# Performance work log

Measured on AMD Instinct MI355X. Metric: run time of the kernel, lower is better.

Reference implementation:

```python
import jax, jax.numpy as jnp
import numpy as np
from jax import lax

B, L, LQ, D_IN, ET, H, INIT_EMBED = 16, 256, 64, 32, 128, 4, 8
DIM = 2 * D_IN          # attention value/feature dim (x concat mask)
ETK = ET // H           # per-head time-embedding dim


def _lin(key, fan_in, shape):
    b = 1.0 / np.sqrt(fan_in)
    return jax.random.uniform(key, shape, jnp.float32, -b, b)


def setup_inputs() -> dict:
    key = jax.random.key(0)
    ks = jax.random.split(key, 24)
    inp = {
        "x": jax.random.normal(ks[0], (B, L, D_IN), jnp.float32),
        "time_steps": jnp.sort(jax.random.uniform(ks[1], (B, L), jnp.float32), axis=-1),
        "mask": (jax.random.uniform(ks[2], (B, L, D_IN)) > 0.5).astype(jnp.float32),
        "query": jnp.linspace(0.0, 1.0, LQ, dtype=jnp.float32),
        # time embedding: Linear(1,1) and Linear(1, ET-1)
        "w_lin": _lin(ks[3], 1, (1,)), "b_lin": _lin(ks[4], 1, (1,)),
        "w_per": _lin(ks[5], 1, (ET - 1,)), "b_per": _lin(ks[6], 1, (ET - 1,)),
        # attention projections (stored as (in,out))
        "Wq": _lin(ks[7], ET, (ET, ET)), "bq": _lin(ks[8], ET, (ET,)),
        "Wk": _lin(ks[9], ET, (ET, ET)), "bk": _lin(ks[10], ET, (ET,)),
        "Wo": _lin(ks[11], H * DIM, (H * DIM, ET)), "bo": _lin(ks[12], H * DIM, (ET,)),
        # vanilla RNN (tanh)
        "W_ih": _lin(ks[13], ET, (ET, ET)), "b_ih": _lin(ks[14], ET, (ET,)),
        "W_hh": _lin(ks[15], ET, (ET, ET)), "b_hh": _lin(ks[16], ET, (ET,)),
        "r1_w": _lin(ks[17], ET, (ET, 128)), "r1_b": _lin(ks[17], ET, (128,)),
        "r2_w": _lin(ks[18], 128, (128, 128)), "r2_b": _lin(ks[18], 128, (128,)),
        "r3_w": _lin(ks[19], 128, (128, ET)), "r3_b": _lin(ks[19], 128, (ET,)),
        "r4_w": _lin(ks[20], ET, (ET, INIT_EMBED)), "r4_b": _lin(ks[20], ET, (INIT_EMBED,)),
    }
    return inp


def reference(x, time_steps, mask, query,
              w_lin, b_lin, w_per, b_per,
              Wq, bq, Wk, bk, Wo, bo,
              W_ih, b_ih, W_hh, b_hh,
              r1_w, r1_b, r2_w, r2_b, r3_w, r3_b, r4_w, r4_b):
    def time_embed(tt):  # (...,) -> (..., ET)
        tt = tt[..., None]
        return jnp.concatenate([tt * w_lin + b_lin,
                                jnp.sin(tt * w_per + b_per)], axis=-1)

    xc = jnp.concatenate([x, mask], axis=-1)          # (B,L,DIM) value
    m2 = jnp.concatenate([mask, mask], axis=-1)       # (B,L,DIM)

    kemb = time_embed(time_steps)                     # (B,L,ET)
    qemb = time_embed(query)                          # (LQ,ET)

    q = (qemb @ Wq + bq).reshape(LQ, H, ETK).transpose(1, 0, 2)       # (H,LQ,ETK)
    k = (kemb @ Wk + bk).reshape(B, L, H, ETK).transpose(0, 2, 1, 3)  # (B,H,L,ETK)

    scores = jnp.einsum('hqe,bhke->bhqk', q, k) / np.sqrt(ETK)        # (B,H,LQ,L)
    # per-feature mask broadcast: (B,H,LQ,L,DIM)
    s5 = jnp.where(m2[:, None, None, :, :] == 0, -1e9, scores[..., None])
    p = jax.nn.softmax(s5, axis=-2)                   # softmax over keys L
    att = jnp.einsum('bhqkd,bkd->bhqd', p, xc)        # (B,H,LQ,DIM)
    att = att.transpose(0, 2, 1, 3).reshape(B, LQ, H * DIM)
    out = att @ Wo + bo                               # (B,LQ,ET)

    # vanilla tanh RNN, return final hidden state
    def step(h, xt):
        h = jnp.tanh(xt @ W_ih + b_ih + h @ W_hh + b_hh)
        return h, None
    h0 = jnp.zeros((B, ET), out.dtype)
    hT, _ = lax.scan(step, h0, out.transpose(1, 0, 2))  # scan over LQ

    y = hT @ r1_w + r1_b
    y = y @ r2_w + r2_b
    y = y @ r3_w + r3_b
    y = y @ r4_w + r4_b                               # (B, INIT_EMBED)
    return y
```

## Files before the change

### kernel.cpp

```cpp
#include <hip/hip_runtime.h>
#include <hip/hip_bf16.h>


#define NB 16
#define NL 256
#define NLQ 64
#define NDIN 32
#define NET 128
#define NH 4
#define NETK 32

#define HPAD 136
#define PAD(i) ((i) + 4 * ((i) >> 6))

__global__ __launch_bounds__(128) void k_embed_proj(
    const float* __restrict__ ts, const float* __restrict__ query,
    const float* __restrict__ mask,
    const float* __restrict__ w_lin, const float* __restrict__ b_lin,
    const float* __restrict__ w_per, const float* __restrict__ b_per,
    const float* __restrict__ Wk, const float* __restrict__ bk,
    const float* __restrict__ Wq, const float* __restrict__ bq,
    float* __restrict__ kproj, float* __restrict__ qproj,
    unsigned* __restrict__ mbg) {
  __shared__ __align__(16) float emb[8 * NET];
  int g = blockIdx.x;
  int j = threadIdx.x;

  if (g >= 520) {
    int b = g - 520;
#pragma unroll
    for (int half = 0; half < 2; half++) {
      int r = j + 128 * half;
      const float4* mr4 = (const float4*)(mask + (size_t)(b * NL + r) * NDIN);
      unsigned bits = 0;
#pragma unroll
      for (int u = 0; u < 8; u++) {
        float4 m = mr4[u];
        bits |= (m.x != 0.f ? 1u : 0u) << (4 * u);
        bits |= (m.y != 0.f ? 1u : 0u) << (4 * u + 1);
        bits |= (m.z != 0.f ? 1u : 0u) << (4 * u + 2);
        bits |= (m.w != 0.f ? 1u : 0u) << (4 * u + 3);
      }
      mbg[b * NL + r] = bits;
    }
    return;
  }

  bool isQ = (g >= 512);
  int base = (isQ ? g - 512 : g) * 8;
  float wl_ = w_lin[0], bl_ = b_lin[0];
  float wp = (j > 0) ? w_per[j - 1] : 0.f;
  float bp = (j > 0) ? b_per[j - 1] : 0.f;
#pragma unroll
  for (int rr = 0; rr < 8; rr++) {
    float t = isQ ? query[base + rr] : ts[base + rr];
    emb[rr * NET + j] = (j == 0) ? (t * wl_ + bl_) : sinf(t * wp + bp);
  }
  __syncthreads();
  const float* W = isQ ? Wq : Wk;
  float bias = isQ ? bq[j] : bk[j];
  float acc[8];
#pragma unroll
  for (int rr = 0; rr < 8; rr++) acc[rr] = bias;
#pragma unroll 2
  for (int i = 0; i < NET; i += 4) {
    float w0 = W[(size_t)i * NET + j];
    float w1 = W[(size_t)(i + 1) * NET + j];
    float w2 = W[(size_t)(i + 2) * NET + j];
    float w3 = W[(size_t)(i + 3) * NET + j];
#pragma unroll
    for (int rr = 0; rr < 8; rr++) {
      float4 e4 = *(const float4*)&emb[rr * NET + i];
      acc[rr] += e4.x * w0 + e4.y * w1 + e4.z * w2 + e4.w * w3;
    }
  }
  float* dst = isQ ? qproj : kproj;
#pragma unroll
  for (int rr = 0; rr < 8; rr++) dst[(size_t)(base + rr) * NET + j] = acc[rr];
}

__global__ __launch_bounds__(256) void k_attn(
    const float* __restrict__ x, const unsigned* __restrict__ mbg,
    const float* __restrict__ qproj, const float* __restrict__ kproj,
    float* __restrict__ att) {
  const float SC = 0.17677669529663687f;
  int blk = blockIdx.x;
  int qg = blk & 15;
  int h  = (blk >> 4) & 3;
  int b  = blk >> 6;
  int t  = threadIdx.x;

  __shared__ __align__(16) float es4[NL * 4];
  __shared__ float part[3 * 32 * 9];

  {
    int k = t;
    float kr[NETK];
    const float4* kp =
        (const float4*)(kproj + (size_t)(b * NL + k) * NET + h * NETK);
#pragma unroll
    for (int i = 0; i < 8; i++) {
      float4 v = kp[i];
      kr[4 * i] = v.x; kr[4 * i + 1] = v.y;
      kr[4 * i + 2] = v.z; kr[4 * i + 3] = v.w;
    }
    float ev[4];
#pragma unroll
    for (int qq = 0; qq < 4; qq++) {
      const float* qv = qproj + (size_t)(qg * 4 + qq) * NET + h * NETK;
      float s0 = 0.f, s1 = 0.f;
#pragma unroll
      for (int i = 0; i < NETK; i += 2) {
        s0 += qv[i] * kr[i];
        s1 += qv[i + 1] * kr[i + 1];
      }
      ev[qq] = __expf((s0 + s1) * SC);
    }
    *(float4*)&es4[k * 4] = make_float4(ev[0], ev[1], ev[2], ev[3]);
  }
  __syncthreads();

  int kq = t >> 5, c = t & 31;
  float den[4] = {0.f, 0.f, 0.f, 0.f};
  float num[4] = {0.f, 0.f, 0.f, 0.f};
  float sumx = 0.f;
  {
    const float* xb = x + (size_t)b * NL * NDIN;
    const unsigned* mbb = mbg + b * NL;
    int k0 = kq * 32;
#pragma unroll 4
    for (int kk = 0; kk < 32; kk++) {
      int k = k0 + kk;
      float4 e4 = *(const float4*)&es4[k * 4];
      float xv = xb[(size_t)k * NDIN + c];
      float mv = ((mbb[k] >> c) & 1u) ? 1.f : 0.f;
      sumx += xv;
      float e0 = e4.x * mv, e1 = e4.y * mv, e2 = e4.z * mv, e3 = e4.w * mv;
      den[0] += e0; num[0] += e0 * xv;
      den[1] += e1; num[1] += e1 * xv;
      den[2] += e2; num[2] += e2 * xv;
      den[3] += e3; num[3] += e3 * xv;
    }
  }
  sumx += __shfl_xor(sumx, 32, 64);
#pragma unroll
  for (int q = 0; q < 4; q++) {
    den[q] += __shfl_xor(den[q], 32, 64);
    num[q] += __shfl_xor(num[q], 32, 64);
  }
  {
    int w = t >> 6, lane = t & 63;
    if (w > 0 && lane < 32) {
      float* p = &part[((w - 1) * 32 + c) * 9];
#pragma unroll
      for (int q = 0; q < 4; q++) { p[q] = den[q]; p[4 + q] = num[q]; }
      p[8] = sumx;
    }
  }
  __syncthreads();

  if (t < 32) {
#pragma unroll
    for (int ww = 0; ww < 3; ww++) {
      const float* p = &part[(ww * 32 + t) * 9];
#pragma unroll
      for (int q = 0; q < 4; q++) { den[q] += p[q]; num[q] += p[4 + q]; }
      sumx += p[8];
    }
    float meanx = sumx * (1.f / 256.f);
#pragma unroll
    for (int qq = 0; qq < 4; qq++) {
      bool any = (den[qq] > 0.f);
      float* ao =
          att + (size_t)(((b * NLQ + qg * 4 + qq) * NH) + h) * 64;
      ao[t]      = any ? (num[qq] / den[qq]) : meanx;
      ao[32 + t] = any ? 1.f : 0.f;
    }
  }
}

__global__ __launch_bounds__(128) void k_out_xw(
    const float* __restrict__ att,
    const float* __restrict__ Wo, const float* __restrict__ bo,
    const float* __restrict__ Wih, const float* __restrict__ bih,
    const float* __restrict__ bhh, float* __restrict__ XW) {
  int r = blockIdx.x;
  int j = threadIdx.x;
  __shared__ __align__(16) float arow[NH * 64];
  __shared__ __align__(16) float orow[NET];
  arow[j]       = att[(size_t)r * 256 + j];
  arow[j + 128] = att[(size_t)r * 256 + 128 + j];
  __syncthreads();
  float a0 = bo[j], a1 = 0.f, a2 = 0.f, a3 = 0.f;
#pragma unroll 4
  for (int u = 0; u < 256; u += 4) {
    float4 av = *(const float4*)&arow[u];
    a0 += av.x * Wo[(size_t)u * NET + j];
    a1 += av.y * Wo[(size_t)(u + 1) * NET + j];
    a2 += av.z * Wo[(size_t)(u + 2) * NET + j];
    a3 += av.w * Wo[(size_t)(u + 3) * NET + j];
  }
  orow[j] = (a0 + a1) + (a2 + a3);
  __syncthreads();
  float b0 = bih[j] + bhh[j], b1 = 0.f, b2 = 0.f, b3 = 0.f;
#pragma unroll 4
  for (int e = 0; e < NET; e += 4) {
    float4 ov = *(const float4*)&orow[e];
    b0 += ov.x * Wih[(size_t)e * NET + j];
    b1 += ov.y * Wih[(size_t)(e + 1) * NET + j];
    b2 += ov.z * Wih[(size_t)(e + 2) * NET + j];
    b3 += ov.w * Wih[(size_t)(e + 3) * NET + j];
  }
  XW[(size_t)r * NET + j] = (b0 + b1) + (b2 + b3);
}

__device__ __forceinline__ void layer128(const float* src_lds,
                                         const float* __restrict__ W,
                                         const float* __restrict__ bvec,
                                         float* dst_lds, int j, int s) {
  const float4* h4 = (const float4*)(src_lds + s * 68);
  float a0 = 0.f, a1 = 0.f, a2 = 0.f, a3 = 0.f;
#pragma unroll
  for (int i = 0; i < 16; i++) {
    float4 hv = h4[i];
    int base = (s * 64 + 4 * i) * NET + j;
    a0 += hv.x * W[base];
    a1 += hv.y * W[base + NET];
    a2 += hv.z * W[base + 2 * NET];
    a3 += hv.w * W[base + 3 * NET];
  }
  float acc = (a0 + a1) + (a2 + a3);
  acc += __shfl_xor(acc, 1, 64);
  if (s == 0) dst_lds[PAD(j)] = acc + bvec[j];
}

__global__ __launch_bounds__(256, 1) void k_rnn(
    const float* __restrict__ XW, const float* __restrict__ Whh,
    const float* __restrict__ r1w, const float* __restrict__ r1b,
    const float* __restrict__ r2w, const float* __restrict__ r2b,
    const float* __restrict__ r3w, const float* __restrict__ r3b,
    const float* __restrict__ r4w, const float* __restrict__ r4b,
    float* __restrict__ out) {
  int b = blockIdx.x;
  int tid = threadIdx.x;
  int s = tid & 1;
  int j = tid >> 1;
  __shared__ float xwl[NLQ * NET];
  __shared__ float hb[2][HPAD];
  __shared__ float tmp[HPAD];

  {
    const float4* src = (const float4*)(XW + (size_t)b * NLQ * NET);
    float4* dst = (float4*)xwl;
#pragma unroll
    for (int u = 0; u < 8; u++) dst[tid + 256 * u] = src[tid + 256 * u];
  }
  float w[64];
#pragma unroll
  for (int i = 0; i < 64; i++) w[i] = Whh[(s * 64 + i) * NET + j];

  if (tid < 128) hb[0][PAD(tid)] = 0.f;
  __syncthreads();

  for (int t = 0; t < NLQ; t++) {
    float xwv = xwl[t * NET + j];
    const float4* h4 = (const float4*)&hb[t & 1][s * 68];
    float a0 = 0.f, a1 = 0.f, a2 = 0.f, a3 = 0.f;
#pragma unroll
    for (int i = 0; i < 16; i++) {
      float4 hv = h4[i];
      a0 += hv.x * w[4 * i];
      a1 += hv.y * w[4 * i + 1];
      a2 += hv.z * w[4 * i + 2];
      a3 += hv.w * w[4 * i + 3];
    }
    float acc = (a0 + a1) + (a2 + a3);
    acc += __shfl_xor(acc, 1, 64);
    if (s == 0) {
      float z = acc + xwv;
      float e2 = __expf(2.f * z);
      hb[(t + 1) & 1][PAD(j)] = 1.f - 2.f / (e2 + 1.f);
    }
    __syncthreads();
  }

  layer128(hb[0], r1w, r1b, tmp, j, s);
  __syncthreads();
  layer128(tmp, r2w, r2b, hb[1], j, s);
  __syncthreads();
  layer128(hb[1], r3w, r3b, hb[0], j, s);
  __syncthreads();
  if (tid < 64) {
    int jj = tid >> 3, p = tid & 7;
    float y = 0.f;
#pragma unroll
    for (int i = 0; i < 16; i++) {
      int ii = p * 16 + i;
      y += hb[0][PAD(ii)] * r4w[ii * 8 + jj];
    }
    y += __shfl_xor(y, 1, 64);
    y += __shfl_xor(y, 2, 64);
    y += __shfl_xor(y, 4, 64);
    if (p == 0) out[b * 8 + jj] = y + r4b[jj];
  }
}

extern "C" void kernel_launch(void* const* d_in, const int* in_sizes, int n_in,
                              void* d_out, int out_size, void* d_ws, size_t ws_size,
                              hipStream_t stream) {
  const float* x     = (const float*)d_in[0];
  const float* ts    = (const float*)d_in[1];
  const float* mask  = (const float*)d_in[2];
  const float* query = (const float*)d_in[3];
  const float* w_lin = (const float*)d_in[4];
  const float* b_lin = (const float*)d_in[5];
  const float* w_per = (const float*)d_in[6];
  const float* b_per = (const float*)d_in[7];
  const float* Wq    = (const float*)d_in[8];
  const float* bq    = (const float*)d_in[9];
  const float* Wk    = (const float*)d_in[10];
  const float* bk    = (const float*)d_in[11];
  const float* Wo    = (const float*)d_in[12];
  const float* bo    = (const float*)d_in[13];
  const float* Wih   = (const float*)d_in[14];
  const float* bih   = (const float*)d_in[15];
  const float* Whh   = (const float*)d_in[16];
  const float* bhh   = (const float*)d_in[17];
  const float* r1w   = (const float*)d_in[18];
  const float* r1b   = (const float*)d_in[19];
  const float* r2w   = (const float*)d_in[20];
  const float* r2b   = (const float*)d_in[21];
  const float* r3w   = (const float*)d_in[22];
  const float* r3b   = (const float*)d_in[23];
  const float* r4w   = (const float*)d_in[24];
  const float* r4b   = (const float*)d_in[25];
  float* out = (float*)d_out;

  float* ws    = (float*)d_ws;
  float* kproj = ws;
  float* qproj = ws + 524288;
  float* att   = ws + 532480;
  float* XW    = ws + 794624;
  unsigned* mbg = (unsigned*)(ws + 925696);

  k_embed_proj<<<536, 128, 0, stream>>>(
      ts, query, mask, w_lin, b_lin, w_per, b_per, Wk, bk, Wq, bq,
      kproj, qproj, mbg);
  k_attn<<<NB * NH * 16, 256, 0, stream>>>(x, mbg, qproj, kproj, att);
  k_out_xw<<<NB * NLQ, 128, 0, stream>>>(att, Wo, bo, Wih, bih, bhh, XW);
  k_rnn<<<NB, 256, 0, stream>>>(XW, Whh, r1w, r1b, r2w, r2b, r3w, r3b,
                                r4w, r4b, out);
}
```

Baseline: 178.9 us.

## Fuse all stages into one cooperative persistent kernel with grid syncs

Replaces the four-kernel pipeline with a single cooperative kernel that runs embedding/projection, attention plus the output and input-to-hidden projections, and the RNN with the regressor as phases separated by grid.sync. Attention is regrouped per (batch, query) so all heads are done in one block, and the attention output goes straight into the Wo/Wih projections through shared memory, so the att buffer round-trip and the separate k_out_xw launch are gone. The aim is to cut kernel launch gaps and intermediate global traffic. In exchange, the sequential RNN phase runs on only 16 blocks while the rest of the grid sits idle, grid-wide barriers add cost, and each block now recomputes all four heads' scores for its query. The old multi-kernel path is kept as a fallback if the cooperative launch fails.

New measurement: 415.8 us. 2.32x slower.

```diff
diff --git a/kernel.cpp b/kernel.cpp
--- a/kernel.cpp
+++ b/kernel.cpp
@@ -1,5 +1,8 @@
 #include <hip/hip_runtime.h>
 #include <hip/hip_bf16.h>
+#include <hip/hip_cooperative_groups.h>
+
+namespace cg = cooperative_groups;
 
 
 #define NB 16
@@ -12,6 +15,293 @@
 
 #define HPAD 136
 #define PAD(i) ((i) + 4 * ((i) >> 6))
+
+__device__ __forceinline__ void layer128(const float* src_lds,
+                                         const float* __restrict__ W,
+                                         const float* __restrict__ bvec,
+                                         float* dst_lds, int j, int s) {
+  const float4* h4 = (const float4*)(src_lds + s * 68);
+  float a0 = 0.f, a1 = 0.f, a2 = 0.f, a3 = 0.f;
+#pragma unroll
+  for (int i = 0; i < 16; i++) {
+    float4 hv = h4[i];
+    int base = (s * 64 + 4 * i) * NET + j;
+    a0 += hv.x * W[base];
+    a1 += hv.y * W[base + NET];
+    a2 += hv.z * W[base + 2 * NET];
+    a3 += hv.w * W[base + 3 * NET];
+  }
+  float acc = (a0 + a1) + (a2 + a3);
+  acc += __shfl_xor(acc, 1, 64);
+  if (s == 0) dst_lds[PAD(j)] = acc + bvec[j];
+}
+
+__device__ __forceinline__ void embed_unit256(
+    float* emb, const float* __restrict__ tsrc, int base,
+    float wl, float bl, float wp, float bp,
+    const float* __restrict__ W, float bias,
+    float* __restrict__ dst, int t) {
+  int j = t & 127, half = t >> 7;
+  __syncthreads();
+#pragma unroll
+  for (int rr = 0; rr < 4; rr++) {
+    int r = half * 4 + rr;
+    float tv = tsrc[base + r];
+    emb[r * NET + j] = (j == 0) ? (tv * wl + bl) : sinf(tv * wp + bp);
+  }
+  __syncthreads();
+  float acc[4] = {bias, bias, bias, bias};
+#pragma unroll 2
+  for (int i = 0; i < NET; i += 4) {
+    float w0 = W[(size_t)i * NET + j];
+    float w1 = W[(size_t)(i + 1) * NET + j];
+    float w2 = W[(size_t)(i + 2) * NET + j];
+    float w3 = W[(size_t)(i + 3) * NET + j];
+#pragma unroll
+    for (int rr = 0; rr < 4; rr++) {
+      float4 e4 = *(const float4*)&emb[(half * 4 + rr) * NET + i];
+      acc[rr] += e4.x * w0 + e4.y * w1 + e4.z * w2 + e4.w * w3;
+    }
+  }
+#pragma unroll
+  for (int rr = 0; rr < 4; rr++)
+    dst[(size_t)(base + half * 4 + rr) * NET + j] = acc[rr];
+}
+
+__global__ __launch_bounds__(256, 4) void k_mega(
+    const float* __restrict__ x, const float* __restrict__ ts,
+    const float* __restrict__ mask, const float* __restrict__ query,
+    const float* __restrict__ w_lin, const float* __restrict__ b_lin,
+    const float* __restrict__ w_per, const float* __restrict__ b_per,
+    const float* __restrict__ Wq, const float* __restrict__ bq,
+    const float* __restrict__ Wk, const float* __restrict__ bk,
+    const float* __restrict__ Wo, const float* __restrict__ bo,
+    const float* __restrict__ Wih, const float* __restrict__ bih,
+    const float* __restrict__ Whh, const float* __restrict__ bhh,
+    const float* __restrict__ r1w, const float* __restrict__ r1b,
+    const float* __restrict__ r2w, const float* __restrict__ r2b,
+    const float* __restrict__ r3w, const float* __restrict__ r3b,
+    const float* __restrict__ r4w, const float* __restrict__ r4b,
+    float* __restrict__ kproj, float* __restrict__ qproj,
+    float* __restrict__ XW, unsigned* __restrict__ mbg,
+    float* __restrict__ out) {
+  __shared__ __align__(16) float lds[8704];
+  cg::grid_group grid = cg::this_grid();
+  int blk = blockIdx.x;
+  int nblk = gridDim.x;
+  int t = threadIdx.x;
+
+  {
+    int j = t & 127;
+    float wl = w_lin[0], bl = b_lin[0];
+    float wp = (j > 0) ? w_per[j - 1] : 0.f;
+    float bp = (j > 0) ? b_per[j - 1] : 0.f;
+    for (int u = blk; u < 536; u += nblk) {
+      if (u < 512) {
+        embed_unit256(lds, ts, u * 8, wl, bl, wp, bp, Wk, bk[j], kproj, t);
+      } else if (u < 520) {
+        embed_unit256(lds, query, (u - 512) * 8, wl, bl, wp, bp, Wq, bq[j],
+                      qproj, t);
+      } else {
+        int b = u - 520;
+        const float4* mr4 =
+            (const float4*)(mask + (size_t)(b * NL + t) * NDIN);
+        unsigned bits = 0;
+#pragma unroll
+        for (int v = 0; v < 8; v++) {
+          float4 m = mr4[v];
+          bits |= (m.x != 0.f ? 1u : 0u) << (4 * v);
+          bits |= (m.y != 0.f ? 1u : 0u) << (4 * v + 1);
+          bits |= (m.z != 0.f ? 1u : 0u) << (4 * v + 2);
+          bits |= (m.w != 0.f ? 1u : 0u) << (4 * v + 3);
+        }
+        mbg[b * NL + t] = bits;
+      }
+    }
+  }
+  grid.sync();
+
+  {
+    const float SC = 0.17677669529663687f;
+    float* es   = lds;
+    float* part = lds + 1024;
+    float* arow = lds + 1920;
+    float* orow = lds + 2176;
+    for (int u = blk; u < NB * NLQ; u += nblk) {
+      __syncthreads();
+      int b = u >> 6, q = u & 63;
+      {
+        int k = t;
+        const float* kpr = kproj + (size_t)(b * NL + k) * NET;
+        float ev[NH];
+#pragma unroll
+        for (int h = 0; h < NH; h++) {
+          float kr[NETK];
+          const float4* kp = (const float4*)(kpr + h * NETK);
+#pragma unroll
+          for (int i = 0; i < 8; i++) {
+            float4 v = kp[i];
+            kr[4 * i] = v.x; kr[4 * i + 1] = v.y;
+            kr[4 * i + 2] = v.z; kr[4 * i + 3] = v.w;
+          }
+          const float* qv = qproj + (size_t)q * NET + h * NETK;
+          float s0 = 0.f, s1 = 0.f;
+#pragma unroll
+          for (int i = 0; i < NETK; i += 2) {
+            s0 += qv[i] * kr[i];
+            s1 += qv[i + 1] * kr[i + 1];
+          }
+          ev[h] = __expf((s0 + s1) * SC);
+        }
+        *(float4*)&es[k * 4] = make_float4(ev[0], ev[1], ev[2], ev[3]);
+      }
+      __syncthreads();
+      float den[NH] = {0.f, 0.f, 0.f, 0.f};
+      float num[NH] = {0.f, 0.f, 0.f, 0.f};
+      float sumx = 0.f;
+      int c = t & 31;
+      {
+        int kq = t >> 5;
+        const float* xb = x + (size_t)b * NL * NDIN;
+        const unsigned* mbb = mbg + b * NL;
+        int k0 = kq * 32;
+#pragma unroll 4
+        for (int kk = 0; kk < 32; kk++) {
+          int k = k0 + kk;
+          float4 e4 = *(const float4*)&es[k * 4];
+          float xv = xb[(size_t)k * NDIN + c];
+          float mv = ((mbb[k] >> c) & 1u) ? 1.f : 0.f;
+          sumx += xv;
+          float e0 = e4.x * mv, e1 = e4.y * mv, e2 = e4.z * mv, e3 = e4.w * mv;
+          den[0] += e0; num[0] += e0 * xv;
+          den[1] += e1; num[1] += e1 * xv;
+          den[2] += e2; num[2] += e2 * xv;
+          den[3] += e3; num[3] += e3 * xv;
+        }
+      }
+      sumx += __shfl_xor(sumx, 32, 64);
+#pragma unroll
+      for (int hh = 0; hh < NH; hh++) {
+        den[hh] += __shfl_xor(den[hh], 32, 64);
+        num[hh] += __shfl_xor(num[hh], 32, 64);
+      }
+      {
+        int w = t >> 6, l = t & 63;
+        if (w > 0 && l < 32) {
+          float* p = &part[((w - 1) * 32 + c) * 9];
+#pragma unroll
+          for (int hh = 0; hh < NH; hh++) { p[hh] = den[hh]; p[4 + hh] = num[hh]; }
+          p[8] = sumx;
+        }
+      }
+      __syncthreads();
+      if (t < 32) {
+#pragma unroll
+        for (int ww = 0; ww < 3; ww++) {
+          const float* p = &part[(ww * 32 + t) * 9];
+#pragma unroll
+          for (int hh = 0; hh < NH; hh++) { den[hh] += p[hh]; num[hh] += p[4 + hh]; }
+          sumx += p[8];
+        }
+        float meanx = sumx * (1.f / 256.f);
+#pragma unroll
+        for (int hh = 0; hh < NH; hh++) {
+          bool any = (den[hh] > 0.f);
+          arow[hh * 64 + t]      = any ? (num[hh] / den[hh]) : meanx;
+          arow[hh * 64 + 32 + t] = any ? 1.f : 0.f;
+        }
+      }
+      __syncthreads();
+      if (t < 128) {
+        float o0 = bo[t], o1 = 0.f, o2 = 0.f, o3 = 0.f;
+#pragma unroll 4
+        for (int uu = 0; uu < 256; uu += 4) {
+          float4 av = *(const float4*)&arow[uu];
+          o0 += av.x * Wo[(size_t)uu * NET + t];
+          o1 += av.y * Wo[(size_t)(uu + 1) * NET + t];
+          o2 += av.z * Wo[(size_t)(uu + 2) * NET + t];
+          o3 += av.w * Wo[(size_t)(uu + 3) * NET + t];
+        }
+        orow[t] = (o0 + o1) + (o2 + o3);
+      }
+      __syncthreads();
+      if (t < 128) {
+        float a0 = bih[t] + bhh[t], a1 = 0.f, a2 = 0.f, a3 = 0.f;
+#pragma unroll 4
+        for (int e = 0; e < NET; e += 4) {
+          float4 ov = *(const float4*)&orow[e];
+          a0 += ov.x * Wih[(size_t)e * NET + t];
+          a1 += ov.y * Wih[(size_t)(e + 1) * NET + t];
+          a2 += ov.z * Wih[(size_t)(e + 2) * NET + t];
+          a3 += ov.w * Wih[(size_t)(e + 3) * NET + t];
+        }
+        XW[(size_t)(b * NLQ + q) * NET + t] = (a0 + a1) + (a2 + a3);
+      }
+    }
+  }
+  grid.sync();
+
+  for (int b = blk; b < NB; b += nblk) {
+    float* xwl = lds;
+    float* hb0 = lds + 8192;
+    float* hb1 = lds + 8192 + HPAD;
+    float* tmp = lds + 8192 + 2 * HPAD;
+    int s = t & 1, j = t >> 1;
+    {
+      const float4* src = (const float4*)(XW + (size_t)b * NLQ * NET);
+      float4* dst = (float4*)xwl;
+#pragma unroll
+      for (int v = 0; v < 8; v++) dst[t + 256 * v] = src[t + 256 * v];
+    }
+    float w[64];
+#pragma unroll
+    for (int i = 0; i < 64; i++) w[i] = Whh[(s * 64 + i) * NET + j];
+    if (t < 128) hb0[PAD(t)] = 0.f;
+    __syncthreads();
+    for (int tt = 0; tt < NLQ; tt++) {
+      float xwv = xwl[tt * NET + j];
+      const float* hsrc = (tt & 1) ? hb1 : hb0;
+      const float4* h4 = (const float4*)&hsrc[s * 68];
+      float a0 = 0.f, a1 = 0.f, a2 = 0.f, a3 = 0.f;
+#pragma unroll
+      for (int i = 0; i < 16; i++) {
+        float4 hv = h4[i];
+        a0 += hv.x * w[4 * i];
+        a1 += hv.y * w[4 * i + 1];
+        a2 += hv.z * w[4 * i + 2];
+        a3 += hv.w * w[4 * i + 3];
+      }
+      float acc = (a0 + a1) + (a2 + a3);
+      acc += __shfl_xor(acc, 1, 64);
+      if (s == 0) {
+        float z = acc + xwv;
+        float e2 = __expf(2.f * z);
+        float* hdst = (tt & 1) ? hb0 : hb1;
+        hdst[PAD(j)] = 1.f - 2.f / (e2 + 1.f);
+      }
+      __syncthreads();
+    }
+    layer128(hb0, r1w, r1b, tmp, j, s);
+    __syncthreads();
+    layer128(tmp, r2w, r2b, hb1, j, s);
+    __syncthreads();
+    layer128(hb1, r3w, r3b, hb0, j, s);
+    __syncthreads();
+    if (t < 64) {
+      int jj = t >> 3, p = t & 7;
+      float y = 0.f;
+#pragma unroll
+      for (int i = 0; i < 16; i++) {
+        int ii = p * 16 + i;
+        y += hb0[PAD(ii)] * r4w[ii * 8 + jj];
+      }
+      y += __shfl_xor(y, 1, 64);
+      y += __shfl_xor(y, 2, 64);
+      y += __shfl_xor(y, 4, 64);
+      if (p == 0) out[b * 8 + jj] = y + r4b[jj];
+    }
+  }
+}
 
 __global__ __launch_bounds__(128) void k_embed_proj(
     const float* __restrict__ ts, const float* __restrict__ query,
@@ -25,7 +315,6 @@
   __shared__ __align__(16) float emb[8 * NET];
   int g = blockIdx.x;
   int j = threadIdx.x;
-
   if (g >= 520) {
     int b = g - 520;
 #pragma unroll
@@ -45,7 +334,6 @@
     }
     return;
   }
-
   bool isQ = (g >= 512);
   int base = (isQ ? g - 512 : g) * 8;
   float wl_ = w_lin[0], bl_ = b_lin[0];
@@ -89,10 +377,8 @@
   int h  = (blk >> 4) & 3;
   int b  = blk >> 6;
   int t  = threadIdx.x;
-
   __shared__ __align__(16) float es4[NL * 4];
   __shared__ float part[3 * 32 * 9];
-
   {
     int k = t;
     float kr[NETK];
@@ -119,7 +405,6 @@
     *(float4*)&es4[k * 4] = make_float4(ev[0], ev[1], ev[2], ev[3]);
   }
   __syncthreads();
-
   int kq = t >> 5, c = t & 31;
   float den[4] = {0.f, 0.f, 0.f, 0.f};
   float num[4] = {0.f, 0.f, 0.f, 0.f};
@@ -158,7 +443,6 @@
     }
   }
   __syncthreads();
-
   if (t < 32) {
 #pragma unroll
     for (int ww = 0; ww < 3; ww++) {
@@ -171,8 +455,7 @@
 #pragma unroll
     for (int qq = 0; qq < 4; qq++) {
       bool any = (den[qq] > 0.f);
-      float* ao =
-          att + (size_t)(((b * NLQ + qg * 4 + qq) * NH) + h) * 64;
+      float* ao = att + (size_t)(((b * NLQ + qg * 4 + qq) * NH) + h) * 64;
       ao[t]      = any ? (num[qq] / den[qq]) : meanx;
       ao[32 + t] = any ? 1.f : 0.f;
     }
@@ -212,26 +495,6 @@
     b3 += ov.w * Wih[(size_t)(e + 3) * NET + j];
   }
   XW[(size_t)r * NET + j] = (b0 + b1) + (b2 + b3);
-}
-
-__device__ __forceinline__ void layer128(const float* src_lds,
-                                         const float* __restrict__ W,
-                                         const float* __restrict__ bvec,
-                                         float* dst_lds, int j, int s) {
-  const float4* h4 = (const float4*)(src_lds + s * 68);
-  float a0 = 0.f, a1 = 0.f, a2 = 0.f, a3 = 0.f;
-#pragma unroll
-  for (int i = 0; i < 16; i++) {
-    float4 hv = h4[i];
-    int base = (s * 64 + 4 * i) * NET + j;
-    a0 += hv.x * W[base];
-    a1 += hv.y * W[base + NET];
-    a2 += hv.z * W[base + 2 * NET];
-    a3 += hv.w * W[base + 3 * NET];
-  }
-  float acc = (a0 + a1) + (a2 + a3);
-  acc += __shfl_xor(acc, 1, 64);
-  if (s == 0) dst_lds[PAD(j)] = acc + bvec[j];
 }
 
 __global__ __launch_bounds__(256, 1) void k_rnn(
@@ -248,7 +511,6 @@
   __shared__ float xwl[NLQ * NET];
   __shared__ float hb[2][HPAD];
   __shared__ float tmp[HPAD];
-
   {
     const float4* src = (const float4*)(XW + (size_t)b * NLQ * NET);
     float4* dst = (float4*)xwl;
@@ -258,10 +520,8 @@
   float w[64];
 #pragma unroll
   for (int i = 0; i < 64; i++) w[i] = Whh[(s * 64 + i) * NET + j];
-
   if (tid < 128) hb[0][PAD(tid)] = 0.f;
   __syncthreads();
-
   for (int t = 0; t < NLQ; t++) {
     float xwv = xwl[t * NET + j];
     const float4* h4 = (const float4*)&hb[t & 1][s * 68];
@@ -283,7 +543,6 @@
     }
     __syncthreads();
   }
-
   layer128(hb[0], r1w, r1b, tmp, j, s);
   __syncthreads();
   layer128(tmp, r2w, r2b, hb[1], j, s);
@@ -339,9 +598,37 @@
   float* ws    = (float*)d_ws;
   float* kproj = ws;
   float* qproj = ws + 524288;
-  float* att   = ws + 532480;
-  float* XW    = ws + 794624;
-  unsigned* mbg = (unsigned*)(ws + 925696);
+  float* XW    = ws + 532480;
+  unsigned* mbg = (unsigned*)(ws + 663552);
+  float* att   = ws + 667648;
+
+  static int coop_state = 0;
+  static int nblk = 1024;
+  if (coop_state == 0) {
+    int mpc = 0;
+    if (hipOccupancyMaxActiveBlocksPerMultiprocessor(
+            &mpc, (const void*)k_mega, 256, 0) != hipSuccess || mpc < 1)
+      mpc = 1;
+    long nb = (long)mpc * 256;
+    nblk = (int)(nb > 1024 ? 1024 : nb);
+    coop_state = 1;
+  }
+  if (coop_state == 1) {
+    void* args[] = {
+        (void*)&x,   (void*)&ts,  (void*)&mask, (void*)&query,
+        (void*)&w_lin, (void*)&b_lin, (void*)&w_per, (void*)&b_per,
+        (void*)&Wq,  (void*)&bq,  (void*)&Wk,  (void*)&bk,
+        (void*)&Wo,  (void*)&bo,  (void*)&Wih, (void*)&bih,
+        (void*)&Whh, (void*)&bhh,
+        (void*)&r1w, (void*)&r1b, (void*)&r2w, (void*)&r2b,
+        (void*)&r3w, (void*)&r3b, (void*)&r4w, (void*)&r4b,
+        (void*)&kproj, (void*)&qproj, (void*)&XW, (void*)&mbg,
+        (void*)&out};
+    hipError_t e = hipLaunchCooperativeKernel(
+        (const void*)k_mega, dim3(nblk), dim3(256), args, 0, stream);
+    if (e == hipSuccess) return;
+    coop_state = -1;
+  }
 
   k_embed_proj<<<536, 128, 0, stream>>>(
       ts, query, mask, w_lin, b_lin, w_per, b_per, Wk, bk, Wq, bq,
```

## Fuse attention with output and input projections, remapping blocks to (batch, query)

Applied to the files above, without the earlier changes.

Attention and the Wo/W_ih projection kernel are merged into one kernel. Each block now handles one (batch, query) pair across all four heads instead of four queries for one head, so the attention row lands in shared memory and feeds the two GEMVs directly. This removes one kernel launch and the global round trip of the att buffer, and both GEMVs split their reduction across 256 threads. The cost is fewer queries per block, so each key row is reloaded once per query and the Wo/Wih weights are read by all 1024 blocks.

Measured after the change: 190.0 us. +6.2%, slower.

```diff
diff --git a/kernel.cpp b/kernel.cpp
--- a/kernel.cpp
+++ b/kernel.cpp
@@ -25,7 +25,6 @@
   __shared__ __align__(16) float emb[8 * NET];
   int g = blockIdx.x;
   int j = threadIdx.x;
-
   if (g >= 520) {
     int b = g - 520;
 #pragma unroll
@@ -45,7 +44,6 @@
     }
     return;
   }
-
   bool isQ = (g >= 512);
   int base = (isQ ? g - 512 : g) * 8;
   float wl_ = w_lin[0], bl_ = b_lin[0];
@@ -79,59 +77,64 @@
   for (int rr = 0; rr < 8; rr++) dst[(size_t)(base + rr) * NET + j] = acc[rr];
 }
 
-__global__ __launch_bounds__(256) void k_attn(
+__global__ __launch_bounds__(256) void k_attn_oxw(
     const float* __restrict__ x, const unsigned* __restrict__ mbg,
     const float* __restrict__ qproj, const float* __restrict__ kproj,
-    float* __restrict__ att) {
+    const float* __restrict__ Wo, const float* __restrict__ bo,
+    const float* __restrict__ Wih, const float* __restrict__ bih,
+    const float* __restrict__ bhh, float* __restrict__ XW) {
   const float SC = 0.17677669529663687f;
-  int blk = blockIdx.x;
-  int qg = blk & 15;
-  int h  = (blk >> 4) & 3;
-  int b  = blk >> 6;
-  int t  = threadIdx.x;
-
-  __shared__ __align__(16) float es4[NL * 4];
+  int u = blockIdx.x;
+  int b = u >> 6, q = u & 63;
+  int t = threadIdx.x;
+
+  __shared__ __align__(16) float es[NL * 4];
   __shared__ float part[3 * 32 * 9];
+  __shared__ __align__(16) float arow[256];
+  __shared__ float po[2][NET];
+  __shared__ __align__(16) float orow[NET];
+  __shared__ float pw[2][NET];
 
   {
     int k = t;
-    float kr[NETK];
-    const float4* kp =
-        (const float4*)(kproj + (size_t)(b * NL + k) * NET + h * NETK);
-#pragma unroll
-    for (int i = 0; i < 8; i++) {
-      float4 v = kp[i];
-      kr[4 * i] = v.x; kr[4 * i + 1] = v.y;
-      kr[4 * i + 2] = v.z; kr[4 * i + 3] = v.w;
-    }
-    float ev[4];
-#pragma unroll
-    for (int qq = 0; qq < 4; qq++) {
-      const float* qv = qproj + (size_t)(qg * 4 + qq) * NET + h * NETK;
+    const float* kpr = kproj + (size_t)(b * NL + k) * NET;
+    float ev[NH];
+#pragma unroll
+    for (int h = 0; h < NH; h++) {
+      float kr[NETK];
+      const float4* kp = (const float4*)(kpr + h * NETK);
+#pragma unroll
+      for (int i = 0; i < 8; i++) {
+        float4 v = kp[i];
+        kr[4 * i] = v.x; kr[4 * i + 1] = v.y;
+        kr[4 * i + 2] = v.z; kr[4 * i + 3] = v.w;
+      }
+      const float* qv = qproj + (size_t)q * NET + h * NETK;
       float s0 = 0.f, s1 = 0.f;
 #pragma unroll
       for (int i = 0; i < NETK; i += 2) {
         s0 += qv[i] * kr[i];
         s1 += qv[i + 1] * kr[i + 1];
       }
-      ev[qq] = __expf((s0 + s1) * SC);
-    }
-    *(float4*)&es4[k * 4] = make_float4(ev[0], ev[1], ev[2], ev[3]);
-  }
-  __syncthreads();
-
-  int kq = t >> 5, c = t & 31;
-  float den[4] = {0.f, 0.f, 0.f, 0.f};
-  float num[4] = {0.f, 0.f, 0.f, 0.f};
+      ev[h] = __expf((s0 + s1) * SC);
+    }
+    *(float4*)&es[k * 4] = make_float4(ev[0], ev[1], ev[2], ev[3]);
+  }
+  __syncthreads();
+
+  float den[NH] = {0.f, 0.f, 0.f, 0.f};
+  float num[NH] = {0.f, 0.f, 0.f, 0.f};
   float sumx = 0.f;
-  {
+  int c = t & 31;
+  {
+    int kq = t >> 5;
     const float* xb = x + (size_t)b * NL * NDIN;
     const unsigned* mbb = mbg + b * NL;
     int k0 = kq * 32;
 #pragma unroll 4
     for (int kk = 0; kk < 32; kk++) {
       int k = k0 + kk;
-      float4 e4 = *(const float4*)&es4[k * 4];
+      float4 e4 = *(const float4*)&es[k * 4];
       float xv = xb[(size_t)k * NDIN + c];
       float mv = ((mbb[k] >> c) & 1u) ? 1.f : 0.f;
       sumx += xv;
@@ -144,74 +147,74 @@
   }
   sumx += __shfl_xor(sumx, 32, 64);
 #pragma unroll
-  for (int q = 0; q < 4; q++) {
-    den[q] += __shfl_xor(den[q], 32, 64);
-    num[q] += __shfl_xor(num[q], 32, 64);
-  }
-  {
-    int w = t >> 6, lane = t & 63;
-    if (w > 0 && lane < 32) {
+  for (int hh = 0; hh < NH; hh++) {
+    den[hh] += __shfl_xor(den[hh], 32, 64);
+    num[hh] += __shfl_xor(num[hh], 32, 64);
+  }
+  {
+    int w = t >> 6, l = t & 63;
+    if (w > 0 && l < 32) {
       float* p = &part[((w - 1) * 32 + c) * 9];
 #pragma unroll
-      for (int q = 0; q < 4; q++) { p[q] = den[q]; p[4 + q] = num[q]; }
+      for (int hh = 0; hh < NH; hh++) { p[hh] = den[hh]; p[4 + hh] = num[hh]; }
       p[8] = sumx;
     }
   }
   __syncthreads();
-
   if (t < 32) {
 #pragma unroll
     for (int ww = 0; ww < 3; ww++) {
       const float* p = &part[(ww * 32 + t) * 9];
 #pragma unroll
-      for (int q = 0; q < 4; q++) { den[q] += p[q]; num[q] += p[4 + q]; }
+      for (int hh = 0; hh < NH; hh++) { den[hh] += p[hh]; num[hh] += p[4 + hh]; }
       sumx += p[8];
     }
     float meanx = sumx * (1.f / 256.f);
 #pragma unroll
-    for (int qq = 0; qq < 4; qq++) {
-      bool any = (den[qq] > 0.f);
-      float* ao =
-          att + (size_t)(((b * NLQ + qg * 4 + qq) * NH) + h) * 64;
-      ao[t]      = any ? (num[qq] / den[qq]) : meanx;
-      ao[32 + t] = any ? 1.f : 0.f;
-    }
-  }
-}
-
-__global__ __launch_bounds__(128) void k_out_xw(
-    const float* __restrict__ att,
-    const float* __restrict__ Wo, const float* __restrict__ bo,
-    const float* __restrict__ Wih, const float* __restrict__ bih,
-    const float* __restrict__ bhh, float* __restrict__ XW) {
-  int r = blockIdx.x;
-  int j = threadIdx.x;
-  __shared__ __align__(16) float arow[NH * 64];
-  __shared__ __align__(16) float orow[NET];
-  arow[j]       = att[(size_t)r * 256 + j];
-  arow[j + 128] = att[(size_t)r * 256 + 128 + j];
-  __syncthreads();
-  float a0 = bo[j], a1 = 0.f, a2 = 0.f, a3 = 0.f;
+    for (int hh = 0; hh < NH; hh++) {
+      bool any = (den[hh] > 0.f);
+      arow[hh * 64 + t]      = any ? (num[hh] / den[hh]) : meanx;
+      arow[hh * 64 + 32 + t] = any ? 1.f : 0.f;
+    }
+  }
+  __syncthreads();
+
+  {
+    int j = t & 127, half = t >> 7;
+    int u0 = half * 128;
+    float o0 = 0.f, o1 = 0.f, o2 = 0.f, o3 = 0.f;
 #pragma unroll 4
-  for (int u = 0; u < 256; u += 4) {
-    float4 av = *(const float4*)&arow[u];
-    a0 += av.x * Wo[(size_t)u * NET + j];
-    a1 += av.y * Wo[(size_t)(u + 1) * NET + j];
-    a2 += av.z * Wo[(size_t)(u + 2) * NET + j];
-    a3 += av.w * Wo[(size_t)(u + 3) * NET + j];
-  }
-  orow[j] = (a0 + a1) + (a2 + a3);
-  __syncthreads();
-  float b0 = bih[j] + bhh[j], b1 = 0.f, b2 = 0.f, b3 = 0.f;
+    for (int uu = u0; uu < u0 + 128; uu += 4) {
+      float4 av = *(const float4*)&arow[uu];
+      o0 += av.x * Wo[(size_t)uu * NET + j];
+      o1 += av.y * Wo[(size_t)(uu + 1) * NET + j];
+      o2 += av.z * Wo[(size_t)(uu + 2) * NET + j];
+      o3 += av.w * Wo[(size_t)(uu + 3) * NET + j];
+    }
+    po[half][j] = (o0 + o1) + (o2 + o3);
+  }
+  __syncthreads();
+  if (t < 128) orow[t] = po[0][t] + po[1][t] + bo[t];
+  __syncthreads();
+
+  {
+    int j = t & 127, half = t >> 7;
+    int e0 = half * 64;
+    float a0 = 0.f, a1 = 0.f, a2 = 0.f, a3 = 0.f;
 #pragma unroll 4
-  for (int e = 0; e < NET; e += 4) {
-    float4 ov = *(const float4*)&orow[e];
-    b0 += ov.x * Wih[(size_t)e * NET + j];
-    b1 += ov.y * Wih[(size_t)(e + 1) * NET + j];
-    b2 += ov.z * Wih[(size_t)(e + 2) * NET + j];
-    b3 += ov.w * Wih[(size_t)(e + 3) * NET + j];
-  }
-  XW[(size_t)r * NET + j] = (b0 + b1) + (b2 + b3);
+    for (int e = e0; e < e0 + 64; e += 4) {
+      float4 ov = *(const float4*)&orow[e];
+      a0 += ov.x * Wih[(size_t)e * NET + j];
+      a1 += ov.y * Wih[(size_t)(e + 1) * NET + j];
+      a2 += ov.z * Wih[(size_t)(e + 2) * NET + j];
+      a3 += ov.w * Wih[(size_t)(e + 3) * NET + j];
+    }
+    pw[half][j] = (a0 + a1) + (a2 + a3);
+  }
+  __syncthreads();
+  if (t < 128)
+    XW[(size_t)(b * NLQ + q) * NET + t] =
+        pw[0][t] + pw[1][t] + bih[t] + bhh[t];
 }
 
 __device__ __forceinline__ void layer128(const float* src_lds,
@@ -248,7 +251,6 @@
   __shared__ float xwl[NLQ * NET];
   __shared__ float hb[2][HPAD];
   __shared__ float tmp[HPAD];
-
   {
     const float4* src = (const float4*)(XW + (size_t)b * NLQ * NET);
     float4* dst = (float4*)xwl;
@@ -258,10 +260,8 @@
   float w[64];
 #pragma unroll
   for (int i = 0; i < 64; i++) w[i] = Whh[(s * 64 + i) * NET + j];
-
   if (tid < 128) hb[0][PAD(tid)] = 0.f;
   __syncthreads();
-
   for (int t = 0; t < NLQ; t++) {
     float xwv = xwl[t * NET + j];
     const float4* h4 = (const float4*)&hb[t & 1][s * 68];
@@ -283,7 +283,6 @@
     }
     __syncthreads();
   }
-
   layer128(hb[0], r1w, r1b, tmp, j, s);
   __syncthreads();
   layer128(tmp, r2w, r2b, hb[1], j, s);
@@ -339,15 +338,14 @@
   float* ws    = (float*)d_ws;
   float* kproj = ws;
   float* qproj = ws + 524288;
-  float* att   = ws + 532480;
-  float* XW    = ws + 794624;
-  unsigned* mbg = (unsigned*)(ws + 925696);
+  float* XW    = ws + 532480;
+  unsigned* mbg = (unsigned*)(ws + 663552);
 
   k_embed_proj<<<536, 128, 0, stream>>>(
       ts, query, mask, w_lin, b_lin, w_per, b_per, Wk, bk, Wq, bq,
       kproj, qproj, mbg);
-  k_attn<<<NB * NH * 16, 256, 0, stream>>>(x, mbg, qproj, kproj, att);
-  k_out_xw<<<NB * NLQ, 128, 0, stream>>>(att, Wo, bo, Wih, bih, bhh, XW);
+  k_attn_oxw<<<NB * NLQ, 256, 0, stream>>>(
+      x, mbg, qproj, kproj, Wo, bo, Wih, bih, bhh, XW);
   k_rnn<<<NB, 256, 0, stream>>>(XW, Whh, r1w, r1b, r2w, r2b, r3w, r3b,
                                 r4w, r4b, out);
 }
```
